# Optimization experiments

Hardware: AMD Instinct MI355X
Metric: run time of the kernel (lower is better)

Reference implementation:

```python
import jax, jax.numpy as jnp
import numpy as np

N_GC = 8192
N_PC = 2048
PF_FANIN = 256
BATCH = 4096


def _build_mask(seed=0):
    # Matches torch logic: per Purkinje cell, pick pf_fanin random granule cells.
    rng = np.random.default_rng(seed)
    mask = np.zeros((N_PC, N_GC), dtype=np.float32)
    for p in range(N_PC):
        idx = rng.permutation(N_GC)[:PF_FANIN]
        mask[p, idx] = 1.0
    return jnp.asarray(mask)


def setup_inputs() -> dict:
    key = jax.random.key(0)
    k1, k2 = jax.random.split(key)
    g_in = jax.random.normal(k1, (BATCH, N_GC), dtype=jnp.float32)
    # kaiming_uniform-ish init for raw weights
    bound = 1.0 / np.sqrt(N_GC)
    W_raw = jax.random.uniform(k2, (N_PC, N_GC), dtype=jnp.float32, minval=-bound, maxval=bound)
    b_pc = jnp.zeros((N_PC,), dtype=jnp.float32)
    mask = _build_mask(0)
    return {"g_in": g_in, "W_raw": W_raw, "b_pc": b_pc, "mask": mask}


def reference(g_in, W_raw, b_pc, mask):
    # effective weight: softplus(W_raw) * mask, shape [n_pc, n_gc]
    W = jax.nn.softplus(W_raw) * mask
    # pc = relu(g_in @ W.T + b)  -> [batch, n_pc]
    pc = jnp.einsum('bg,pg->bp', g_in, W) + b_pc
    return jax.nn.relu(pc)
```

## Files before the change

### kernel.cpp

```cpp
#include <hip/hip_runtime.h>

#define BATCH 4096
#define NGC   8192
#define NPC   2048

typedef _Float16 f16;
typedef __attribute__((ext_vector_type(8))) _Float16 f16x8;
typedef __attribute__((ext_vector_type(4))) _Float16 f16x4;
typedef __attribute__((ext_vector_type(4))) float   floatx4;

__device__ __forceinline__ float softplus_f(float x) {
    return fmaxf(x, 0.0f) + log1pf(expf(-fabsf(x)));
}

__global__ void cvt_g(const float* __restrict__ g, f16* __restrict__ gh) {
    int i = (blockIdx.x * blockDim.x + threadIdx.x) * 4;
    float4 v = *(const float4*)(g + i);
    f16x4 h;
    h[0] = (f16)v.x; h[1] = (f16)v.y; h[2] = (f16)v.z; h[3] = (f16)v.w;
    *(f16x4*)(gh + i) = h;
}

__global__ void cvt_w(const float* __restrict__ W, const float* __restrict__ mask,
                      f16* __restrict__ wh) {
    int i = (blockIdx.x * blockDim.x + threadIdx.x) * 4;
    float4 w = *(const float4*)(W + i);
    float4 m = *(const float4*)(mask + i);
    f16x4 h;
    h[0] = (f16)(softplus_f(w.x) * m.x);
    h[1] = (f16)(softplus_f(w.y) * m.y);
    h[2] = (f16)(softplus_f(w.z) * m.z);
    h[3] = (f16)(softplus_f(w.w) * m.w);
    *(f16x4*)(wh + i) = h;
}

__device__ __forceinline__ void gload_lds16(const f16* g, f16* l) {
    __builtin_amdgcn_global_load_lds((const __attribute__((address_space(1))) void*)g,
                                     (__attribute__((address_space(3))) void*)l,
                                     16, 0, 0);
}

__global__ void gemm_f16(const f16* __restrict__ A, const f16* __restrict__ B,
                         const float* __restrict__ bias, float* __restrict__ out) {
    __shared__ __align__(16) f16 As[128 * 64];
    __shared__ __align__(16) f16 Bs[128 * 64];

    const int tid  = threadIdx.x;
    const int lane = tid & 63;
    const int wid  = tid >> 6;
    const int bm0  = blockIdx.y * 128;
    const int bn0  = blockIdx.x * 128;
    const int wm   = (wid >> 1) * 64;
    const int wn   = (wid & 1) * 64;
    const int l15  = lane & 15;
    const int lq   = lane >> 4;

    floatx4 acc[4][4] = {};

    for (int kt = 0; kt < NGC / 64; ++kt) {
        const int k0 = kt * 64;
        __syncthreads();
#pragma unroll
        for (int i = 0; i < 4; ++i) {
            int d = tid + 256 * i;
            int r = d >> 3;
            int g = (d & 7) ^ (r & 7);
            gload_lds16(A + (size_t)(bm0 + r) * NGC + k0 + g * 8, As + d * 8);
            gload_lds16(B + (size_t)(bn0 + r) * NGC + k0 + g * 8, Bs + d * 8);
        }
        __syncthreads();
#pragma unroll
        for (int ks = 0; ks < 2; ++ks) {
            const int g = ks * 4 + lq;
            f16x8 a[4], b[4];
#pragma unroll
            for (int t = 0; t < 4; ++t) {
                int ra = wm + t * 16 + l15;
                int ca = (ra << 3) | (g ^ (ra & 7));
                a[t] = *(const f16x8*)(As + ca * 8);
                int rb = wn + t * 16 + l15;
                int cb = (rb << 3) | (g ^ (rb & 7));
                b[t] = *(const f16x8*)(Bs + cb * 8);
            }
#pragma unroll
            for (int mt = 0; mt < 4; ++mt)
#pragma unroll
                for (int nt = 0; nt < 4; ++nt)
                    acc[mt][nt] = __builtin_amdgcn_mfma_f32_16x16x32_f16(
                        a[mt], b[nt], acc[mt][nt], 0, 0, 0);
        }
    }

#pragma unroll
    for (int nt = 0; nt < 4; ++nt) {
        int col  = bn0 + wn + nt * 16 + l15;
        float bv = bias[col];
#pragma unroll
        for (int mt = 0; mt < 4; ++mt) {
#pragma unroll
            for (int r = 0; r < 4; ++r) {
                int row = bm0 + wm + mt * 16 + lq * 4 + r;
                float x = acc[mt][nt][r] + bv;
                out[(size_t)row * NPC + col] = fmaxf(x, 0.0f);
            }
        }
    }
}

__global__ void naive_kernel(const float* __restrict__ g, const float* __restrict__ W,
                             const float* __restrict__ bias, const float* __restrict__ mask,
                             float* __restrict__ out) {
    int idx = blockIdx.x * 256 + threadIdx.x;
    int b = idx / NPC, p = idx % NPC;
    const float* gr = g + (size_t)b * NGC;
    const float* wr = W + (size_t)p * NGC;
    const float* mr = mask + (size_t)p * NGC;
    float acc = bias[p];
    for (int k = 0; k < NGC; ++k) {
        float m = mr[k];
        if (m != 0.0f) acc += gr[k] * softplus_f(wr[k]);
    }
    out[idx] = fmaxf(acc, 0.0f);
}

extern "C" void kernel_launch(void* const* d_in, const int* in_sizes, int n_in,
                              void* d_out, int out_size, void* d_ws, size_t ws_size,
                              hipStream_t stream) {
    const float* g_in  = (const float*)d_in[0];
    const float* W_raw = (const float*)d_in[1];
    const float* b_pc  = (const float*)d_in[2];
    const float* mask  = (const float*)d_in[3];
    float* out = (float*)d_out;

    const size_t gh_elems = (size_t)BATCH * NGC;
    const size_t wh_elems = (size_t)NPC * NGC;
    const size_t need = (gh_elems + wh_elems) * sizeof(f16);

    if (ws_size >= need) {
        f16* gh = (f16*)d_ws;
        f16* wh = gh + gh_elems;
        cvt_g<<<(int)(gh_elems / 1024), 256, 0, stream>>>(g_in, gh);
        cvt_w<<<(int)(wh_elems / 1024), 256, 0, stream>>>(W_raw, mask, wh);
        dim3 grid(NPC / 128, BATCH / 128);
        gemm_f16<<<grid, 256, 0, stream>>>(gh, wh, b_pc, out);
    } else {
        naive_kernel<<<BATCH * NPC / 256, 256, 0, stream>>>(g_in, W_raw, b_pc, mask, out);
    }
}
```

Measured before the change: 447.1 us.

## Fuse conversion kernels and shrink GEMM M-tile to 64 for more blocks

Merges the g and W conversion kernels into a single launch that processes 8 elements per thread. Halves the GEMM block tile in M from 128 to 64, doubling the grid to improve CU occupancy and tail balance. Smaller tiles reduce data reuse per block and raise load traffic per MFMA.

```diff
diff --git a/kernel.cpp b/kernel.cpp
--- a/kernel.cpp
+++ b/kernel.cpp
@@ -6,32 +6,45 @@
 
 typedef _Float16 f16;
 typedef __attribute__((ext_vector_type(8))) _Float16 f16x8;
-typedef __attribute__((ext_vector_type(4))) _Float16 f16x4;
 typedef __attribute__((ext_vector_type(4))) float   floatx4;
 
 __device__ __forceinline__ float softplus_f(float x) {
     return fmaxf(x, 0.0f) + log1pf(expf(-fabsf(x)));
 }
 
-__global__ void cvt_g(const float* __restrict__ g, f16* __restrict__ gh) {
-    int i = (blockIdx.x * blockDim.x + threadIdx.x) * 4;
-    float4 v = *(const float4*)(g + i);
-    f16x4 h;
-    h[0] = (f16)v.x; h[1] = (f16)v.y; h[2] = (f16)v.z; h[3] = (f16)v.w;
-    *(f16x4*)(gh + i) = h;
-}
+#define G_ELEMS (BATCH * NGC)
+#define W_ELEMS (NPC * NGC)
+#define G_BLOCKS (G_ELEMS / 2048)
+#define W_BLOCKS (W_ELEMS / 2048)
 
-__global__ void cvt_w(const float* __restrict__ W, const float* __restrict__ mask,
-                      f16* __restrict__ wh) {
-    int i = (blockIdx.x * blockDim.x + threadIdx.x) * 4;
-    float4 w = *(const float4*)(W + i);
-    float4 m = *(const float4*)(mask + i);
-    f16x4 h;
-    h[0] = (f16)(softplus_f(w.x) * m.x);
-    h[1] = (f16)(softplus_f(w.y) * m.y);
-    h[2] = (f16)(softplus_f(w.z) * m.z);
-    h[3] = (f16)(softplus_f(w.w) * m.w);
-    *(f16x4*)(wh + i) = h;
+__global__ void cvt_all(const float* __restrict__ g, const float* __restrict__ W,
+                        const float* __restrict__ mask,
+                        f16* __restrict__ gh, f16* __restrict__ wh) {
+    if (blockIdx.x < G_BLOCKS) {
+        size_t i = (size_t)blockIdx.x * 2048 + threadIdx.x * 8;
+        float4 v0 = *(const float4*)(g + i);
+        float4 v1 = *(const float4*)(g + i + 4);
+        f16x8 h;
+        h[0] = (f16)v0.x; h[1] = (f16)v0.y; h[2] = (f16)v0.z; h[3] = (f16)v0.w;
+        h[4] = (f16)v1.x; h[5] = (f16)v1.y; h[6] = (f16)v1.z; h[7] = (f16)v1.w;
+        *(f16x8*)(gh + i) = h;
+    } else {
+        size_t i = (size_t)(blockIdx.x - G_BLOCKS) * 2048 + threadIdx.x * 8;
+        float4 w0 = *(const float4*)(W + i);
+        float4 w1 = *(const float4*)(W + i + 4);
+        float4 m0 = *(const float4*)(mask + i);
+        float4 m1 = *(const float4*)(mask + i + 4);
+        f16x8 h;
+        h[0] = (f16)(softplus_f(w0.x) * m0.x);
+        h[1] = (f16)(softplus_f(w0.y) * m0.y);
+        h[2] = (f16)(softplus_f(w0.z) * m0.z);
+        h[3] = (f16)(softplus_f(w0.w) * m0.w);
+        h[4] = (f16)(softplus_f(w1.x) * m1.x);
+        h[5] = (f16)(softplus_f(w1.y) * m1.y);
+        h[6] = (f16)(softplus_f(w1.z) * m1.z);
+        h[7] = (f16)(softplus_f(w1.w) * m1.w);
+        *(f16x8*)(wh + i) = h;
+    }
 }
 
 __device__ __forceinline__ void gload_lds16(const f16* g, f16* l) {
@@ -42,48 +55,57 @@
 
 __global__ void gemm_f16(const f16* __restrict__ A, const f16* __restrict__ B,
                          const float* __restrict__ bias, float* __restrict__ out) {
-    __shared__ __align__(16) f16 As[128 * 64];
+    __shared__ __align__(16) f16 As[64 * 64];
     __shared__ __align__(16) f16 Bs[128 * 64];
 
     const int tid  = threadIdx.x;
     const int lane = tid & 63;
     const int wid  = tid >> 6;
-    const int bm0  = blockIdx.y * 128;
+    const int bm0  = blockIdx.y * 64;
     const int bn0  = blockIdx.x * 128;
-    const int wm   = (wid >> 1) * 64;
+    const int wm   = (wid >> 1) * 32;
     const int wn   = (wid & 1) * 64;
     const int l15  = lane & 15;
     const int lq   = lane >> 4;
 
-    floatx4 acc[4][4] = {};
+    floatx4 acc[2][4] = {};
 
     for (int kt = 0; kt < NGC / 64; ++kt) {
         const int k0 = kt * 64;
         __syncthreads();
 #pragma unroll
+        for (int i = 0; i < 2; ++i) {
+            int d = tid + 256 * i;
+            int r = d >> 3;
+            int g = (d & 7) ^ (r & 7);
+            gload_lds16(A + (size_t)(bm0 + r) * NGC + k0 + g * 8, As + d * 8);
+        }
+#pragma unroll
         for (int i = 0; i < 4; ++i) {
             int d = tid + 256 * i;
             int r = d >> 3;
             int g = (d & 7) ^ (r & 7);
-            gload_lds16(A + (size_t)(bm0 + r) * NGC + k0 + g * 8, As + d * 8);
             gload_lds16(B + (size_t)(bn0 + r) * NGC + k0 + g * 8, Bs + d * 8);
         }
         __syncthreads();
 #pragma unroll
         for (int ks = 0; ks < 2; ++ks) {
             const int g = ks * 4 + lq;
-            f16x8 a[4], b[4];
+            f16x8 a[2], b[4];
 #pragma unroll
-            for (int t = 0; t < 4; ++t) {
+            for (int t = 0; t < 2; ++t) {
                 int ra = wm + t * 16 + l15;
                 int ca = (ra << 3) | (g ^ (ra & 7));
                 a[t] = *(const f16x8*)(As + ca * 8);
+            }
+#pragma unroll
+            for (int t = 0; t < 4; ++t) {
                 int rb = wn + t * 16 + l15;
                 int cb = (rb << 3) | (g ^ (rb & 7));
                 b[t] = *(const f16x8*)(Bs + cb * 8);
             }
 #pragma unroll
-            for (int mt = 0; mt < 4; ++mt)
+            for (int mt = 0; mt < 2; ++mt)
 #pragma unroll
                 for (int nt = 0; nt < 4; ++nt)
                     acc[mt][nt] = __builtin_amdgcn_mfma_f32_16x16x32_f16(
@@ -96,7 +118,7 @@
         int col  = bn0 + wn + nt * 16 + l15;
         float bv = bias[col];
 #pragma unroll
-        for (int mt = 0; mt < 4; ++mt) {
+        for (int mt = 0; mt < 2; ++mt) {
 #pragma unroll
             for (int r = 0; r < 4; ++r) {
                 int row = bm0 + wm + mt * 16 + lq * 4 + r;
@@ -132,16 +154,15 @@
     const float* mask  = (const float*)d_in[3];
     float* out = (float*)d_out;
 
-    const size_t gh_elems = (size_t)BATCH * NGC;
-    const size_t wh_elems = (size_t)NPC * NGC;
+    const size_t gh_elems = (size_t)G_ELEMS;
+    const size_t wh_elems = (size_t)W_ELEMS;
     const size_t need = (gh_elems + wh_elems) * sizeof(f16);
 
     if (ws_size >= need) {
         f16* gh = (f16*)d_ws;
         f16* wh = gh + gh_elems;
-        cvt_g<<<(int)(gh_elems / 1024), 256, 0, stream>>>(g_in, gh);
-        cvt_w<<<(int)(wh_elems / 1024), 256, 0, stream>>>(W_raw, mask, wh);
-        dim3 grid(NPC / 128, BATCH / 128);
+        cvt_all<<<G_BLOCKS + W_BLOCKS, 256, 0, stream>>>(g_in, W_raw, mask, gh, wh);
+        dim3 grid(NPC / 128, BATCH / 64);
         gemm_f16<<<grid, 256, 0, stream>>>(gh, wh, b_pc, out);
     } else {
         naive_kernel<<<BATCH * NPC / 256, 256, 0, stream>>>(g_in, W_raw, b_pc, mask, out);
```

New measurement: 468.2 us. 1.05x slower.

## Fuse activation fp32-to-fp16 conversion into GEMM LDS load path

Applied to the files above, without the earlier changes.

Drops the separate cvt_g kernel and has the GEMM load fp32 activations straight into LDS through a 16-column XOR swizzle. Each tile is converted to fp16 when fragments are read from LDS. This removes a full pass that wrote and re-read a 64MB fp16 copy, but doubles the A-tile LDS footprint and global traffic inside the GEMM and adds conversion ALU work in the inner loop. The weight conversion kernel is also widened to eight elements per thread.

```diff
diff --git a/kernel.cpp b/kernel.cpp
--- a/kernel.cpp
+++ b/kernel.cpp
@@ -6,44 +6,44 @@
 
 typedef _Float16 f16;
 typedef __attribute__((ext_vector_type(8))) _Float16 f16x8;
-typedef __attribute__((ext_vector_type(4))) _Float16 f16x4;
 typedef __attribute__((ext_vector_type(4))) float   floatx4;
 
 __device__ __forceinline__ float softplus_f(float x) {
     return fmaxf(x, 0.0f) + log1pf(expf(-fabsf(x)));
 }
 
-__global__ void cvt_g(const float* __restrict__ g, f16* __restrict__ gh) {
-    int i = (blockIdx.x * blockDim.x + threadIdx.x) * 4;
-    float4 v = *(const float4*)(g + i);
-    f16x4 h;
-    h[0] = (f16)v.x; h[1] = (f16)v.y; h[2] = (f16)v.z; h[3] = (f16)v.w;
-    *(f16x4*)(gh + i) = h;
-}
+#define W_ELEMS (NPC * NGC)
+#define W_BLOCKS (W_ELEMS / 2048)
 
 __global__ void cvt_w(const float* __restrict__ W, const float* __restrict__ mask,
                       f16* __restrict__ wh) {
-    int i = (blockIdx.x * blockDim.x + threadIdx.x) * 4;
-    float4 w = *(const float4*)(W + i);
-    float4 m = *(const float4*)(mask + i);
-    f16x4 h;
-    h[0] = (f16)(softplus_f(w.x) * m.x);
-    h[1] = (f16)(softplus_f(w.y) * m.y);
-    h[2] = (f16)(softplus_f(w.z) * m.z);
-    h[3] = (f16)(softplus_f(w.w) * m.w);
-    *(f16x4*)(wh + i) = h;
+    size_t i = (size_t)blockIdx.x * 2048 + threadIdx.x * 8;
+    float4 w0 = *(const float4*)(W + i);
+    float4 w1 = *(const float4*)(W + i + 4);
+    float4 m0 = *(const float4*)(mask + i);
+    float4 m1 = *(const float4*)(mask + i + 4);
+    f16x8 h;
+    h[0] = (f16)(softplus_f(w0.x) * m0.x);
+    h[1] = (f16)(softplus_f(w0.y) * m0.y);
+    h[2] = (f16)(softplus_f(w0.z) * m0.z);
+    h[3] = (f16)(softplus_f(w0.w) * m0.w);
+    h[4] = (f16)(softplus_f(w1.x) * m1.x);
+    h[5] = (f16)(softplus_f(w1.y) * m1.y);
+    h[6] = (f16)(softplus_f(w1.z) * m1.z);
+    h[7] = (f16)(softplus_f(w1.w) * m1.w);
+    *(f16x8*)(wh + i) = h;
 }
 
-__device__ __forceinline__ void gload_lds16(const f16* g, f16* l) {
+__device__ __forceinline__ void gload_lds16(const void* g, void* l) {
     __builtin_amdgcn_global_load_lds((const __attribute__((address_space(1))) void*)g,
                                      (__attribute__((address_space(3))) void*)l,
                                      16, 0, 0);
 }
 
-__global__ void gemm_f16(const f16* __restrict__ A, const f16* __restrict__ B,
+__global__ void gemm_f16(const float* __restrict__ A, const f16* __restrict__ B,
                          const float* __restrict__ bias, float* __restrict__ out) {
-    __shared__ __align__(16) f16 As[128 * 64];
-    __shared__ __align__(16) f16 Bs[128 * 64];
+    __shared__ __align__(16) float Asf[128 * 64];
+    __shared__ __align__(16) f16   Bs [128 * 64];
 
     const int tid  = threadIdx.x;
     const int lane = tid & 63;
@@ -60,24 +60,41 @@
     for (int kt = 0; kt < NGC / 64; ++kt) {
         const int k0 = kt * 64;
         __syncthreads();
+
+#pragma unroll
+        for (int i = 0; i < 8; ++i) {
+            int d = tid + 256 * i;
+            int r = d >> 4;
+            int c = (d & 15) ^ (r & 15);
+            gload_lds16(A + (size_t)(bm0 + r) * NGC + k0 + c * 4, Asf + d * 4);
+        }
 #pragma unroll
         for (int i = 0; i < 4; ++i) {
             int d = tid + 256 * i;
             int r = d >> 3;
             int g = (d & 7) ^ (r & 7);
-            gload_lds16(A + (size_t)(bm0 + r) * NGC + k0 + g * 8, As + d * 8);
             gload_lds16(B + (size_t)(bn0 + r) * NGC + k0 + g * 8, Bs + d * 8);
         }
         __syncthreads();
+
 #pragma unroll
         for (int ks = 0; ks < 2; ++ks) {
             const int g = ks * 4 + lq;
             f16x8 a[4], b[4];
 #pragma unroll
             for (int t = 0; t < 4; ++t) {
-                int ra = wm + t * 16 + l15;
-                int ca = (ra << 3) | (g ^ (ra & 7));
-                a[t] = *(const f16x8*)(As + ca * 8);
+                int ra  = wm + t * 16 + l15;
+                int dA0 = (ra << 4) | ((2 * g)     ^ (ra & 15));
+                int dA1 = (ra << 4) | ((2 * g + 1) ^ (ra & 15));
+                floatx4 lo = *(const floatx4*)(Asf + dA0 * 4);
+                floatx4 hi = *(const floatx4*)(Asf + dA1 * 4);
+                f16x8 av;
+                av[0] = (f16)lo[0]; av[1] = (f16)lo[1];
+                av[2] = (f16)lo[2]; av[3] = (f16)lo[3];
+                av[4] = (f16)hi[0]; av[5] = (f16)hi[1];
+                av[6] = (f16)hi[2]; av[7] = (f16)hi[3];
+                a[t] = av;
+
                 int rb = wn + t * 16 + l15;
                 int cb = (rb << 3) | (g ^ (rb & 7));
                 b[t] = *(const f16x8*)(Bs + cb * 8);
@@ -132,17 +149,13 @@
     const float* mask  = (const float*)d_in[3];
     float* out = (float*)d_out;
 
-    const size_t gh_elems = (size_t)BATCH * NGC;
-    const size_t wh_elems = (size_t)NPC * NGC;
-    const size_t need = (gh_elems + wh_elems) * sizeof(f16);
+    const size_t need = (size_t)W_ELEMS * sizeof(f16);
 
     if (ws_size >= need) {
-        f16* gh = (f16*)d_ws;
-        f16* wh = gh + gh_elems;
-        cvt_g<<<(int)(gh_elems / 1024), 256, 0, stream>>>(g_in, gh);
-        cvt_w<<<(int)(wh_elems / 1024), 256, 0, stream>>>(W_raw, mask, wh);
+        f16* wh = (f16*)d_ws;
+        cvt_w<<<W_BLOCKS, 256, 0, stream>>>(W_raw, mask, wh);
         dim3 grid(NPC / 128, BATCH / 128);
-        gemm_f16<<<grid, 256, 0, stream>>>(gh, wh, b_pc, out);
+        gemm_f16<<<grid, 256, 0, stream>>>(g_in, wh, b_pc, out);
     } else {
         naive_kernel<<<BATCH * NPC / 256, 256, 0, stream>>>(g_in, W_raw, b_pc, mask, out);
     }
```

Result: slower. 714.4 us (+59.8%).
